# Kernel tuning notes

Measured on AMD Instinct MI355X. Metric: run time of the kernel, lower is better.

The kernel has to match this reference:

```python
import jax, jax.numpy as jnp
import numpy as np

DIM = 512
DIM_INPUTS = (8,)*4 + (16,)*4 + (32,)*4 + (64,)*4 + (128,)*4 + (256,)*4  # 24 bands, sum=2016
N_BANDS = len(DIM_INPUTS)
TOTAL_OUT2 = 2 * sum(DIM_INPUTS)  # 4032 (concatenated last-layer gated width)
B, T = 4, 512


def _glu_tanh(z):
    # LinearGLUWithTanH epilogue: chunk last dim, tanh(a) * sigmoid(gate)
    a, gate = jnp.split(z, 2, axis=-1)
    return jnp.tanh(a) * jax.nn.sigmoid(gate)


def setup_inputs() -> dict:
    key = jax.random.key(0)
    k0, k1, k2, k3, k4 = jax.random.split(key, 5)
    x = jax.random.normal(k0, (B, T, N_BANDS, DIM), dtype=jnp.float32)
    # layer 0: per-band Linear(DIM, 2*DIM), stacked over bands
    W0 = jax.random.normal(k1, (N_BANDS, DIM, 2 * DIM), dtype=jnp.float32) / np.float32(np.sqrt(DIM))
    b0 = jax.random.normal(k2, (N_BANDS, 2 * DIM), dtype=jnp.float32) * 0.01
    # layer 1 (last): per-band Linear(DIM, 2*dim_in); widths differ, so pack
    # all bands' weight columns into one concatenated matrix sliced statically.
    W1 = jax.random.normal(k3, (DIM, TOTAL_OUT2), dtype=jnp.float32) / np.float32(np.sqrt(DIM))
    b1 = jax.random.normal(k4, (TOTAL_OUT2,), dtype=jnp.float32) * 0.01
    return {"x": x, "W0": W0, "b0": b0, "W1": W1, "b1": b1}


def reference(x, W0, b0, W1, b1):
    # layer 0 for all bands in one grouped GEMM: (b t n d),(n d e)->(b t n e)
    h = _glu_tanh(jnp.einsum('btnd,nde->btne', x, W0) + b0)  # (B,T,N,DIM)
    outs = []
    off = 0
    for i, di in enumerate(DIM_INPUTS):  # static loop over structurally distinct bands
        w = W1[:, off:off + 2 * di]
        bb = b1[off:off + 2 * di]
        outs.append(_glu_tanh(h[:, :, i] @ w + bb))  # (B,T,di)
        off += 2 * di
    return jnp.concatenate(outs, axis=-1)  # (B,T,sum(DIM_INPUTS))
```

## Files before the change

kernel.cpp:

```cpp
#include <hip/hip_runtime.h>
#include <cstdint>
#include <cstddef>


typedef _Float16 f16;
typedef _Float16 f16x8 __attribute__((ext_vector_type(8)));
typedef float floatx4 __attribute__((ext_vector_type(4)));

#define BT 2048
#define NB 24

__device__ __forceinline__ int band_di(int b){ return 8 << (b >> 2); }
__device__ __forceinline__ int band_off2(int b){
  int g = b >> 2;
  return 2 * (32 * ((1 << g) - 1) + (b & 3) * (8 << g));
}

__device__ __forceinline__ float fsigm(float x){
  return __builtin_amdgcn_rcpf(1.f + __expf(-x));
}
__device__ __forceinline__ float ftanh(float x){
  return 1.f - 2.f * __builtin_amdgcn_rcpf(1.f + __expf(2.f * x));
}

__device__ __forceinline__ void gl_lds16(const void* g, void* l){
  __builtin_amdgcn_global_load_lds(
      (const __attribute__((address_space(1))) unsigned int*)g,
      (__attribute__((address_space(3))) unsigned int*)l, 16, 0, 0);
}


__global__ __launch_bounds__(256) void cast_x(const float4* __restrict__ in,
                                              f16* __restrict__ out){
  int t = blockIdx.x * 256 + threadIdx.x;
  float4 v = in[t];
  typedef _Float16 f16x4 __attribute__((ext_vector_type(4)));
  f16x4 o = { (f16)v.x, (f16)v.y, (f16)v.z, (f16)v.w };
  *(f16x4*)(out + (size_t)t * 4) = o;
}

__global__ __launch_bounds__(256) void cast_w0(const float* __restrict__ W0,
                                               f16* __restrict__ w0t){
  __shared__ float tile[64][33];
  int bid = blockIdx.x;
  int dt   = bid & 7;
  int half = (bid >> 3) & 1;
  int g    = (bid >> 4) & 15;
  int band = bid >> 8;
  int t = threadIdx.x;
  int c0 = half * 512 + g * 32;
  int d0 = dt * 64;
  int r  = t >> 2;
  int cs = (t & 3) * 8;
  const float* src = W0 + ((size_t)(band * 512 + d0 + r)) * 1024 + c0 + cs;
  float4 v0 = *(const float4*)src;
  float4 v1 = *(const float4*)(src + 4);
  tile[r][cs + 0] = v0.x; tile[r][cs + 1] = v0.y; tile[r][cs + 2] = v0.z; tile[r][cs + 3] = v0.w;
  tile[r][cs + 4] = v1.x; tile[r][cs + 5] = v1.y; tile[r][cs + 6] = v1.z; tile[r][cs + 7] = v1.w;
  __syncthreads();
  int i   = t >> 3;
  int ds8 = (t & 7) * 8;
  int prow = g * 64 + 2 * i + half;
  f16x8 o;
  #pragma unroll
  for (int k = 0; k < 8; ++k) o[k] = (f16)tile[ds8 + k][i];
  *(f16x8*)(w0t + ((size_t)(band * 1024 + prow)) * 512 + d0 + ds8) = o;
}

__global__ __launch_bounds__(256) void cast_w1(const float* __restrict__ W1,
                                               f16* __restrict__ w1t){
  __shared__ f16 tile[16][520];
  int jt = blockIdx.x;
  int j16 = jt * 16;
  int band = 23;
  for (int b = 0; b < 24; ++b){ if (j16 < band_off2(b + 1)) { band = b; break; } }
  int off2 = band_off2(band), di = band_di(band);
  int p0 = j16 - off2;
  int oca = off2 + (p0 >> 1);
  int ocg = oca + di;
  int t = threadIdx.x;
  #pragma unroll
  for (int hh = 0; hh < 2; ++hh){
    int d = hh * 256 + t;
    const float* rowp = W1 + (size_t)d * 4032;
    float4 a0 = *(const float4*)(rowp + oca);
    float4 a1 = *(const float4*)(rowp + oca + 4);
    float4 g0 = *(const float4*)(rowp + ocg);
    float4 g1 = *(const float4*)(rowp + ocg + 4);
    float av[8] = {a0.x,a0.y,a0.z,a0.w,a1.x,a1.y,a1.z,a1.w};
    float gv[8] = {g0.x,g0.y,g0.z,g0.w,g1.x,g1.y,g1.z,g1.w};
    #pragma unroll
    for (int q = 0; q < 8; ++q){
      tile[2*q][d]   = (f16)av[q];
      tile[2*q+1][d] = (f16)gv[q];
    }
  }
  __syncthreads();
  int j = t & 15, dc = (t >> 4) * 32;
  f16x8 o[4];
  #pragma unroll
  for (int k = 0; k < 4; ++k) o[k] = *(const f16x8*)&tile[j][dc + k*8];
  f16* dst = w1t + (size_t)(j16 + j) * 512 + dc;
  #pragma unroll
  for (int k = 0; k < 4; ++k) *(f16x8*)(dst + k*8) = o[k];
}

__global__ __launch_bounds__(256) void cast_bias(const float* __restrict__ b0,
                                                 const float* __restrict__ b1,
                                                 float* __restrict__ b0p,
                                                 float* __restrict__ b1p){
  int t = blockIdx.x * 256 + threadIdx.x;
  if (t < NB * 1024){
    int p = t & 1023;
    int base = t & ~1023;
    b0p[t] = b0[base + ((p & 1) ? 512 + (p >> 1) : (p >> 1))];
  } else {
    int j = t - NB * 1024;
    if (j < 4032){
      int band = 23;
      for (int b = 0; b < 24; ++b){ if (j < band_off2(b + 1)) { band = b; break; } }
      int off2 = band_off2(band);
      int di = band_di(band);
      int p = j - off2;
      b1p[j] = b1[off2 + ((p & 1) ? di + (p >> 1) : (p >> 1))];
    }
  }
}

__global__ __launch_bounds__(256) void gemm1(const f16* __restrict__ xh,
                                             const f16* __restrict__ w0t,
                                             const float* __restrict__ b0p,
                                             f16* __restrict__ h){
  __shared__ __align__(16) f16 As[128 * 64];
  __shared__ __align__(16) f16 Bs[128 * 64];
  int bid = blockIdx.x;
  int wid = (bid & 7) * 384 + (bid >> 3);
  int band = wid >> 7;
  int mt = (wid >> 3) & 15;
  int nt = wid & 7;
  int t = threadIdx.x;
  int lane = t & 63, w = t >> 6;
  int wm = w & 1, wn = w >> 1;
  int quad = lane >> 4, lc = lane & 15;
  const int mrow0 = mt * 128;
  const int nrow0 = nt * 128;

  const char* gA[4]; const char* gB[4];
  f16* lA[4]; f16* lB[4];
  #pragma unroll
  for (int p = 0; p < 4; ++p){
    int idx = p * 256 + t;
    int r = idx >> 3, s = idx & 7, l = s ^ (r & 7);
    gA[p] = (const char*)(xh + ((size_t)(mrow0 + r) * 24 + band) * 512 + l * 8);
    gB[p] = (const char*)(w0t + ((size_t)(band * 1024 + nrow0 + r)) * 512 + l * 8);
    lA[p] = &As[idx * 8];
    lB[p] = &Bs[idx * 8];
  }
  int aoff[4], boff[4];
  #pragma unroll
  for (int i = 0; i < 4; ++i){
    int m = wm * 64 + i * 16 + lc;
    aoff[i] = (m * 64 + ((quad ^ (m & 7)) << 3)) * 2;
    int n = wn * 64 + i * 16 + lc;
    boff[i] = (n * 64 + ((quad ^ (n & 7)) << 3)) * 2;
  }
  const char* Ab = (const char*)As;
  const char* Bb = (const char*)Bs;

  floatx4 acc[4][4];
  #pragma unroll
  for (int i = 0; i < 4; ++i)
    #pragma unroll
    for (int j = 0; j < 4; ++j) acc[i][j] = floatx4{0.f, 0.f, 0.f, 0.f};

  for (int kb = 0; kb < 8; ++kb){
    #pragma unroll
    for (int p = 0; p < 4; ++p){ gl_lds16(gA[p], lA[p]); gA[p] += 128; }
    #pragma unroll
    for (int p = 0; p < 4; ++p){ gl_lds16(gB[p], lB[p]); gB[p] += 128; }
    __syncthreads();
    #pragma unroll
    for (int s2 = 0; s2 < 2; ++s2){
      f16x8 af[4], bf[4];
      #pragma unroll
      for (int i = 0; i < 4; ++i){
        af[i] = *(const f16x8*)(Ab + (aoff[i] ^ (s2 * 64)));
        bf[i] = *(const f16x8*)(Bb + (boff[i] ^ (s2 * 64)));
      }
      #pragma unroll
      for (int i = 0; i < 4; ++i)
        #pragma unroll
        for (int j = 0; j < 4; ++j)
          acc[i][j] = __builtin_amdgcn_mfma_f32_16x16x32_f16(af[i], bf[j], acc[i][j], 0, 0, 0);
    }
    __syncthreads();
  }
  #pragma unroll
  for (int j = 0; j < 4; ++j){
    int colp = nrow0 + wn * 64 + j * 16 + lc;
    float bias = b0p[band * 1024 + colp];
    #pragma unroll
    for (int i = 0; i < 4; ++i){
      int mbase = mrow0 + wm * 64 + i * 16 + quad * 4;
      #pragma unroll
      for (int r = 0; r < 4; ++r){
        float z = acc[i][j][r] + bias;
        float zp = __shfl_xor(z, 1);
        if (!(lc & 1)){
          float hv = ftanh(z) * fsigm(zp);
          h[((size_t)band * BT + mbase + r) * 512 + (colp >> 1)] = (f16)hv;
        }
      }
    }
  }
}

template<int BN>
__device__ __forceinline__ void gemm2_tile(const f16* __restrict__ hb,
                                           const f16* __restrict__ w1t,
                                           const float* __restrict__ b1p,
                                           float* __restrict__ out,
                                           int band, int mt, int ntile,
                                           f16* As, f16* Bs){
  constexpr int WNW = (BN == 128) ? 2 : 1;
  constexpr int WMW = 4 / WNW;
  constexpr int MF = 128 / (WMW * 16);
  constexpr int NF = BN / (WNW * 16);
  int t = threadIdx.x;
  int lane = t & 63, w = t >> 6;
  int wm = (WNW == 2) ? (w & 1) : w;
  int wn = (WNW == 2) ? (w >> 1) : 0;
  int quad = lane >> 4, lc = lane & 15;
  int off2 = band_off2(band);
  int jbase = off2 + ntile * BN;

  constexpr int BCH = BN * 8;
  constexpr int BP = (BCH + 255) / 256;
  const char* gA[4]; const char* gB[BP];
  f16* lA[4]; f16* lB[BP];
  #pragma unroll
  for (int p = 0; p < 4; ++p){
    int idx = p * 256 + t;
    int r = idx >> 3, s = idx & 7, l = s ^ (r & 7);
    gA[p] = (const char*)(hb + ((size_t)(mt * 128 + r)) * 512 + l * 8);
    lA[p] = &As[idx * 8];
  }
  #pragma unroll
  for (int p = 0; p < BP; ++p){
    int idx = p * 256 + t;
    int r = idx >> 3, s = idx & 7, l = s ^ (r & 7);
    gB[p] = (const char*)(w1t + ((size_t)(jbase + r)) * 512 + l * 8);
    lB[p] = &Bs[idx * 8];
  }
  int aoff[MF], boff[NF];
  #pragma unroll
  for (int i = 0; i < MF; ++i){
    int m = wm * (MF * 16) + i * 16 + lc;
    aoff[i] = (m * 64 + ((quad ^ (m & 7)) << 3)) * 2;
  }
  #pragma unroll
  for (int j = 0; j < NF; ++j){
    int n = wn * (NF * 16) + j * 16 + lc;
    boff[j] = (n * 64 + ((quad ^ (n & 7)) << 3)) * 2;
  }
  const char* Ab = (const char*)As;
  const char* Bb = (const char*)Bs;

  floatx4 acc[MF][NF];
  #pragma unroll
  for (int i = 0; i < MF; ++i)
    #pragma unroll
    for (int j = 0; j < NF; ++j) acc[i][j] = floatx4{0.f, 0.f, 0.f, 0.f};

  for (int kb = 0; kb < 8; ++kb){
    #pragma unroll
    for (int p = 0; p < 4; ++p){ gl_lds16(gA[p], lA[p]); gA[p] += 128; }
    #pragma unroll
    for (int p = 0; p < BP; ++p){
      if ((BCH % 256 == 0) || (p * 256 + t) < BCH){
        gl_lds16(gB[p], lB[p]); gB[p] += 128;
      }
    }
    __syncthreads();
    #pragma unroll
    for (int s2 = 0; s2 < 2; ++s2){
      f16x8 af[MF], bf[NF];
      #pragma unroll
      for (int i = 0; i < MF; ++i)
        af[i] = *(const f16x8*)(Ab + (aoff[i] ^ (s2 * 64)));
      #pragma unroll
      for (int j = 0; j < NF; ++j)
        bf[j] = *(const f16x8*)(Bb + (boff[j] ^ (s2 * 64)));
      #pragma unroll
      for (int i = 0; i < MF; ++i)
        #pragma unroll
        for (int j = 0; j < NF; ++j)
          acc[i][j] = __builtin_amdgcn_mfma_f32_16x16x32_f16(af[i], bf[j], acc[i][j], 0, 0, 0);
    }
    __syncthreads();
  }
  int outbase = off2 >> 1;
  #pragma unroll
  for (int j = 0; j < NF; ++j){
    int p = ntile * BN + wn * (NF * 16) + j * 16 + lc;
    float bias = b1p[off2 + p];
    #pragma unroll
    for (int i = 0; i < MF; ++i){
      int mbase = mt * 128 + wm * (MF * 16) + i * 16 + quad * 4;
      #pragma unroll
      for (int r = 0; r < 4; ++r){
        float z = acc[i][j][r] + bias;
        float zp = __shfl_xor(z, 1);
        if (!(lc & 1)){
          out[(size_t)(mbase + r) * 2016 + outbase + (p >> 1)] = ftanh(z) * fsigm(zp);
        }
      }
    }
  }
}

__global__ __launch_bounds__(256) void gemm2(const f16* __restrict__ h,
                                             const f16* __restrict__ w1t,
                                             const float* __restrict__ b1p,
                                             float* __restrict__ out){
  __shared__ __align__(16) f16 As[128 * 64];
  __shared__ __align__(16) f16 Bs[128 * 64];
  int bid = blockIdx.x;
  int band, mt, ntile, cls;
  if (bid < 256){
    band = bid >> 4; mt = bid & 15; ntile = 0; cls = band >> 2;
  } else if (bid < 384){
    int rel = bid - 256; band = 16 + (rel >> 5);
    int r2 = rel & 31; mt = r2 & 15; ntile = r2 >> 4; cls = 4;
  } else {
    int rel = bid - 384; band = 20 + (rel >> 6);
    int r2 = rel & 63; mt = r2 & 15; ntile = r2 >> 4; cls = 5;
  }
  const f16* hb = h + ((size_t)band << 20);
  switch (cls){
    case 0:  gemm2_tile<16 >(hb, w1t, b1p, out, band, mt, ntile, As, Bs); break;
    case 1:  gemm2_tile<32 >(hb, w1t, b1p, out, band, mt, ntile, As, Bs); break;
    case 2:  gemm2_tile<64 >(hb, w1t, b1p, out, band, mt, ntile, As, Bs); break;
    default: gemm2_tile<128>(hb, w1t, b1p, out, band, mt, ntile, As, Bs); break;
  }
}

extern "C" void kernel_launch(void* const* d_in, const int* in_sizes, int n_in,
                              void* d_out, int out_size, void* d_ws, size_t ws_size,
                              hipStream_t stream){
  const float* x  = (const float*)d_in[0];
  const float* W0 = (const float*)d_in[1];
  const float* b0 = (const float*)d_in[2];
  const float* W1 = (const float*)d_in[3];
  const float* b1 = (const float*)d_in[4];
  char* ws = (char*)d_ws;
  f16*   xh   = (f16*)(ws);
  f16*   hbuf = (f16*)(ws + 50331648);
  f16*   w0t  = (f16*)(ws + 100663296);
  f16*   w1t  = (f16*)(ws + 125829120);
  float* b0p  = (float*)(ws + 129957888);
  float* b1p  = (float*)(ws + 130056192);

  cast_x   <<<24576, 256, 0, stream>>>((const float4*)x, xh);
  cast_w0  <<<6144,  256, 0, stream>>>(W0, w0t);
  cast_w1  <<<252,   256, 0, stream>>>(W1, w1t);
  cast_bias<<<112,   256, 0, stream>>>(b0, b1, b0p, b1p);
  gemm1    <<<3072,  256, 0, stream>>>(xh, w0t, b0p, hbuf);
  gemm2    <<<640,   256, 0, stream>>>(hbuf, w1t, b1p, (float*)d_out);
}
```

Before: 317.6 us.

## Fuse cast kernels into one prep launch, band-major x layout, split GLU epilogue

```diff
diff --git a/kernel.cpp b/kernel.cpp
--- a/kernel.cpp
+++ b/kernel.cpp
@@ -29,105 +29,114 @@
       (__attribute__((address_space(3))) unsigned int*)l, 16, 0, 0);
 }
 
-
-__global__ __launch_bounds__(256) void cast_x(const float4* __restrict__ in,
-                                              f16* __restrict__ out){
-  int t = blockIdx.x * 256 + threadIdx.x;
-  float4 v = in[t];
-  typedef _Float16 f16x4 __attribute__((ext_vector_type(4)));
-  f16x4 o = { (f16)v.x, (f16)v.y, (f16)v.z, (f16)v.w };
-  *(f16x4*)(out + (size_t)t * 4) = o;
-}
-
-__global__ __launch_bounds__(256) void cast_w0(const float* __restrict__ W0,
-                                               f16* __restrict__ w0t){
-  __shared__ float tile[64][33];
+__global__ __launch_bounds__(256) void prep(const float* __restrict__ x,
+                                            const float* __restrict__ W0,
+                                            const float* __restrict__ W1,
+                                            const float* __restrict__ b0,
+                                            const float* __restrict__ b1,
+                                            f16* __restrict__ xh2,
+                                            f16* __restrict__ w0t,
+                                            f16* __restrict__ w1t,
+                                            float* __restrict__ b0p,
+                                            float* __restrict__ b1p){
+  __shared__ __align__(16) char smem[33792];
   int bid = blockIdx.x;
-  int dt   = bid & 7;
-  int half = (bid >> 3) & 1;
-  int g    = (bid >> 4) & 15;
-  int band = bid >> 8;
   int t = threadIdx.x;
-  int c0 = half * 512 + g * 32;
-  int d0 = dt * 64;
-  int r  = t >> 2;
-  int cs = (t & 3) * 8;
-  const float* src = W0 + ((size_t)(band * 512 + d0 + r)) * 1024 + c0 + cs;
-  float4 v0 = *(const float4*)src;
-  float4 v1 = *(const float4*)(src + 4);
-  tile[r][cs + 0] = v0.x; tile[r][cs + 1] = v0.y; tile[r][cs + 2] = v0.z; tile[r][cs + 3] = v0.w;
-  tile[r][cs + 4] = v1.x; tile[r][cs + 5] = v1.y; tile[r][cs + 6] = v1.z; tile[r][cs + 7] = v1.w;
-  __syncthreads();
-  int i   = t >> 3;
-  int ds8 = (t & 7) * 8;
-  int prow = g * 64 + 2 * i + half;
-  f16x8 o;
-  #pragma unroll
-  for (int k = 0; k < 8; ++k) o[k] = (f16)tile[ds8 + k][i];
-  *(f16x8*)(w0t + ((size_t)(band * 1024 + prow)) * 512 + d0 + ds8) = o;
-}
-
-__global__ __launch_bounds__(256) void cast_w1(const float* __restrict__ W1,
-                                               f16* __restrict__ w1t){
-  __shared__ f16 tile[16][520];
-  int jt = blockIdx.x;
-  int j16 = jt * 16;
-  int band = 23;
-  for (int b = 0; b < 24; ++b){ if (j16 < band_off2(b + 1)) { band = b; break; } }
-  int off2 = band_off2(band), di = band_di(band);
-  int p0 = j16 - off2;
-  int oca = off2 + (p0 >> 1);
-  int ocg = oca + di;
-  int t = threadIdx.x;
-  #pragma unroll
-  for (int hh = 0; hh < 2; ++hh){
-    int d = hh * 256 + t;
-    const float* rowp = W1 + (size_t)d * 4032;
-    float4 a0 = *(const float4*)(rowp + oca);
-    float4 a1 = *(const float4*)(rowp + oca + 4);
-    float4 g0 = *(const float4*)(rowp + ocg);
-    float4 g1 = *(const float4*)(rowp + ocg + 4);
-    float av[8] = {a0.x,a0.y,a0.z,a0.w,a1.x,a1.y,a1.z,a1.w};
-    float gv[8] = {g0.x,g0.y,g0.z,g0.w,g1.x,g1.y,g1.z,g1.w};
-    #pragma unroll
-    for (int q = 0; q < 8; ++q){
-      tile[2*q][d]   = (f16)av[q];
-      tile[2*q+1][d] = (f16)gv[q];
-    }
-  }
-  __syncthreads();
-  int j = t & 15, dc = (t >> 4) * 32;
-  f16x8 o[4];
-  #pragma unroll
-  for (int k = 0; k < 4; ++k) o[k] = *(const f16x8*)&tile[j][dc + k*8];
-  f16* dst = w1t + (size_t)(j16 + j) * 512 + dc;
-  #pragma unroll
-  for (int k = 0; k < 4; ++k) *(f16x8*)(dst + k*8) = o[k];
-}
-
-__global__ __launch_bounds__(256) void cast_bias(const float* __restrict__ b0,
-                                                 const float* __restrict__ b1,
-                                                 float* __restrict__ b0p,
-                                                 float* __restrict__ b1p){
-  int t = blockIdx.x * 256 + threadIdx.x;
-  if (t < NB * 1024){
-    int p = t & 1023;
-    int base = t & ~1023;
-    b0p[t] = b0[base + ((p & 1) ? 512 + (p >> 1) : (p >> 1))];
+  if (bid < 6144){
+    int r = bid / 3, bg = bid - 3 * r;
+    int band = bg * 8 + (t >> 5);
+    int k16 = (t & 31) * 16;
+    const float* src = x + ((size_t)(r * 24 + band)) * 512 + k16;
+    float4 v0 = *(const float4*)(src + 0);
+    float4 v1 = *(const float4*)(src + 4);
+    float4 v2 = *(const float4*)(src + 8);
+    float4 v3 = *(const float4*)(src + 12);
+    f16x8 o0 = { (f16)v0.x,(f16)v0.y,(f16)v0.z,(f16)v0.w,
+                 (f16)v1.x,(f16)v1.y,(f16)v1.z,(f16)v1.w };
+    f16x8 o1 = { (f16)v2.x,(f16)v2.y,(f16)v2.z,(f16)v2.w,
+                 (f16)v3.x,(f16)v3.y,(f16)v3.z,(f16)v3.w };
+    f16* dst = xh2 + ((size_t)(band * 2048 + r)) * 512 + k16;
+    *(f16x8*)(dst + 0) = o0;
+    *(f16x8*)(dst + 8) = o1;
+  } else if (bid < 12288){
+    float (*tile)[33] = (float(*)[33])smem;
+    int b2 = bid - 6144;
+    int dt   = b2 & 7;
+    int half = (b2 >> 3) & 1;
+    int g    = (b2 >> 4) & 15;
+    int band = b2 >> 8;
+    int c0 = half * 512 + g * 32;
+    int d0 = dt * 64;
+    int r  = t >> 2;
+    int cs = (t & 3) * 8;
+    const float* src = W0 + ((size_t)(band * 512 + d0 + r)) * 1024 + c0 + cs;
+    float4 v0 = *(const float4*)src;
+    float4 v1 = *(const float4*)(src + 4);
+    tile[r][cs+0]=v0.x; tile[r][cs+1]=v0.y; tile[r][cs+2]=v0.z; tile[r][cs+3]=v0.w;
+    tile[r][cs+4]=v1.x; tile[r][cs+5]=v1.y; tile[r][cs+6]=v1.z; tile[r][cs+7]=v1.w;
+    __syncthreads();
+    int i   = t >> 3;
+    int ds8 = (t & 7) * 8;
+    int prow = g * 64 + 2 * i + half;
+    f16x8 o;
+    #pragma unroll
+    for (int k = 0; k < 8; ++k) o[k] = (f16)tile[ds8 + k][i];
+    *(f16x8*)(w0t + ((size_t)(band * 1024 + prow)) * 512 + d0 + ds8) = o;
+  } else if (bid < 12540){
+    f16 (*tw)[520] = (f16(*)[520])smem;
+    int jt = bid - 12288;
+    int j16 = jt * 16;
+    int band = 23;
+    for (int b = 0; b < 24; ++b){ if (j16 < band_off2(b + 1)) { band = b; break; } }
+    int off2 = band_off2(band), di = band_di(band);
+    int p0 = j16 - off2;
+    int oca = off2 + (p0 >> 1);
+    int ocg = oca + di;
+    #pragma unroll
+    for (int hh = 0; hh < 2; ++hh){
+      int d = hh * 256 + t;
+      const float* rowp = W1 + (size_t)d * 4032;
+      float4 a0 = *(const float4*)(rowp + oca);
+      float4 a1 = *(const float4*)(rowp + oca + 4);
+      float4 g0 = *(const float4*)(rowp + ocg);
+      float4 g1 = *(const float4*)(rowp + ocg + 4);
+      float av[8] = {a0.x,a0.y,a0.z,a0.w,a1.x,a1.y,a1.z,a1.w};
+      float gv[8] = {g0.x,g0.y,g0.z,g0.w,g1.x,g1.y,g1.z,g1.w};
+      #pragma unroll
+      for (int q = 0; q < 8; ++q){
+        tw[2*q][d]   = (f16)av[q];
+        tw[2*q+1][d] = (f16)gv[q];
+      }
+    }
+    __syncthreads();
+    int j = t & 15, dc = (t >> 4) * 32;
+    f16x8 o[4];
+    #pragma unroll
+    for (int k = 0; k < 4; ++k) o[k] = *(const f16x8*)&tw[j][dc + k*8];
+    f16* dst = w1t + (size_t)(j16 + j) * 512 + dc;
+    #pragma unroll
+    for (int k = 0; k < 4; ++k) *(f16x8*)(dst + k*8) = o[k];
   } else {
-    int j = t - NB * 1024;
-    if (j < 4032){
-      int band = 23;
-      for (int b = 0; b < 24; ++b){ if (j < band_off2(b + 1)) { band = b; break; } }
-      int off2 = band_off2(band);
-      int di = band_di(band);
-      int p = j - off2;
-      b1p[j] = b1[off2 + ((p & 1) ? di + (p >> 1) : (p >> 1))];
-    }
-  }
-}
-
-__global__ __launch_bounds__(256) void gemm1(const f16* __restrict__ xh,
+    int idx = (bid - 12540) * 256 + t;
+    if (idx < NB * 1024){
+      int p = idx & 1023;
+      int base = idx & ~1023;
+      b0p[idx] = b0[base + ((p & 1) ? 512 + (p >> 1) : (p >> 1))];
+    } else {
+      int j = idx - NB * 1024;
+      if (j < 4032){
+        int band = 23;
+        for (int b = 0; b < 24; ++b){ if (j < band_off2(b + 1)) { band = b; break; } }
+        int off2 = band_off2(band);
+        int di = band_di(band);
+        int p = j - off2;
+        b1p[j] = b1[off2 + ((p & 1) ? di + (p >> 1) : (p >> 1))];
+      }
+    }
+  }
+}
+
+__global__ __launch_bounds__(256) void gemm1(const f16* __restrict__ xh2,
                                              const f16* __restrict__ w0t,
                                              const float* __restrict__ b0p,
                                              f16* __restrict__ h){
@@ -151,7 +160,7 @@
   for (int p = 0; p < 4; ++p){
     int idx = p * 256 + t;
     int r = idx >> 3, s = idx & 7, l = s ^ (r & 7);
-    gA[p] = (const char*)(xh + ((size_t)(mrow0 + r) * 24 + band) * 512 + l * 8);
+    gA[p] = (const char*)(xh2 + ((size_t)(band * 2048 + mrow0 + r)) * 512 + l * 8);
     gB[p] = (const char*)(w0t + ((size_t)(band * 1024 + nrow0 + r)) * 512 + l * 8);
     lA[p] = &As[idx * 8];
     lB[p] = &Bs[idx * 8];
@@ -205,10 +214,10 @@
       #pragma unroll
       for (int r = 0; r < 4; ++r){
         float z = acc[i][j][r] + bias;
-        float zp = __shfl_xor(z, 1);
+        float v = (lc & 1) ? fsigm(z) : ftanh(z);
+        float vp = __shfl_xor(v, 1);
         if (!(lc & 1)){
-          float hv = ftanh(z) * fsigm(zp);
-          h[((size_t)band * BT + mbase + r) * 512 + (colp >> 1)] = (f16)hv;
+          h[((size_t)band * BT + mbase + r) * 512 + (colp >> 1)] = (f16)(v * vp);
         }
       }
     }
@@ -310,9 +319,10 @@
       #pragma unroll
       for (int r = 0; r < 4; ++r){
         float z = acc[i][j][r] + bias;
-        float zp = __shfl_xor(z, 1);
+        float v = (lc & 1) ? fsigm(z) : ftanh(z);
+        float vp = __shfl_xor(v, 1);
         if (!(lc & 1)){
-          out[(size_t)(mbase + r) * 2016 + outbase + (p >> 1)] = ftanh(z) * fsigm(zp);
+          out[(size_t)(mbase + r) * 2016 + outbase + (p >> 1)] = v * vp;
         }
       }
     }
@@ -325,7 +335,8 @@
                                              float* __restrict__ out){
   __shared__ __align__(16) f16 As[128 * 64];
   __shared__ __align__(16) f16 Bs[128 * 64];
-  int bid = blockIdx.x;
+  int bid0 = blockIdx.x;
+  int bid = (bid0 & 7) * 80 + (bid0 >> 3);
   int band, mt, ntile, cls;
   if (bid < 256){
     band = bid >> 4; mt = bid & 15; ntile = 0; cls = band >> 2;
@@ -354,17 +365,14 @@
   const float* W1 = (const float*)d_in[3];
   const float* b1 = (const float*)d_in[4];
   char* ws = (char*)d_ws;
-  f16*   xh   = (f16*)(ws);
+  f16*   xh2  = (f16*)(ws);
   f16*   hbuf = (f16*)(ws + 50331648);
   f16*   w0t  = (f16*)(ws + 100663296);
   f16*   w1t  = (f16*)(ws + 125829120);
   float* b0p  = (float*)(ws + 129957888);
   float* b1p  = (float*)(ws + 130056192);
 
-  cast_x   <<<24576, 256, 0, stream>>>((const float4*)x, xh);
-  cast_w0  <<<6144,  256, 0, stream>>>(W0, w0t);
-  cast_w1  <<<252,   256, 0, stream>>>(W1, w1t);
-  cast_bias<<<112,   256, 0, stream>>>(b0, b1, b0p, b1p);
-  gemm1    <<<3072,  256, 0, stream>>>(xh, w0t, b0p, hbuf);
-  gemm2    <<<640,   256, 0, stream>>>(hbuf, w1t, b1p, (float*)d_out);
-}
+  prep <<<12652, 256, 0, stream>>>(x, W0, W1, b0, b1, xh2, w0t, w1t, b0p, b1p);
+  gemm1<<<3072,  256, 0, stream>>>(xh2, w0t, b0p, hbuf);
+  gemm2<<<640,   256, 0, stream>>>(hbuf, w1t, b1p, (float*)d_out);
+}
```

New measurement: 333.3 us. 1.05x slower.
